# Kernel tuning notes

Hardware: AMD Instinct MI355X
Metric: run time of the kernel (lower is better)

## Reference

```python
import jax, jax.numpy as jnp
import numpy as np

DIM = 1024
HEADS = 16
HEAD_DIM = DIM // HEADS
SCALE = HEADS ** (-0.5)  # NOTE: module scales by heads**-0.5, not head_dim**-0.5


def setup_inputs() -> dict:
    key = jax.random.key(0)
    ks = jax.random.split(key, 5)
    B, N = 4, 2048
    x = jax.random.normal(ks[0], (B, N, DIM), dtype=jnp.float32)
    # qkv: Linear(dim, 3*dim); out: Linear(dim, dim). torch Linear: y = x @ W.T + b
    w_qkv = jax.random.normal(ks[1], (3 * DIM, DIM), dtype=jnp.float32) * (DIM ** -0.5)
    b_qkv = jax.random.normal(ks[2], (3 * DIM,), dtype=jnp.float32) * 0.01
    w_out = jax.random.normal(ks[3], (DIM, DIM), dtype=jnp.float32) * (DIM ** -0.5)
    b_out = jax.random.normal(ks[4], (DIM,), dtype=jnp.float32) * 0.01
    return {"x": x, "w_qkv": w_qkv, "b_qkv": b_qkv, "w_out": w_out, "b_out": b_out}


def reference(x, w_qkv, b_qkv, w_out, b_out):
    B, N, D = x.shape
    qkv = x @ w_qkv.T + b_qkv                       # [B, N, 3D]
    qkv = qkv.reshape(B, N, 3, HEADS, HEAD_DIM)
    qkv = jnp.transpose(qkv, (2, 0, 3, 1, 4))       # [3, B, H, N, hd]
    q, k, v = qkv[0], qkv[1], qkv[2]
    attn = jnp.einsum('bhqd,bhkd->bhqk', q, k) * SCALE
    attn = jax.nn.softmax(attn, axis=-1)
    out = jnp.einsum('bhqk,bhkd->bhqd', attn, v)    # [B, H, N, hd]
    out = jnp.transpose(out, (0, 2, 1, 3)).reshape(B, N, D)
    return out @ w_out.T + b_out
```

## Files before the change

kernel.cpp:

```cpp
#include <hip/hip_runtime.h>
#include <math.h>


typedef float v4f    __attribute__((ext_vector_type(4)));
typedef float f32x16 __attribute__((ext_vector_type(16)));
typedef short s4     __attribute__((ext_vector_type(4)));
typedef short bf8    __attribute__((ext_vector_type(8)));

__device__ __forceinline__ unsigned short bf16r(float f) {
    unsigned int u = __float_as_uint(f);
    u += 0x7FFFu + ((u >> 16) & 1u);
    return (unsigned short)(u >> 16);
}
__device__ __forceinline__ float bf16f(unsigned short h) {
    return __uint_as_float(((unsigned int)h) << 16);
}
__device__ __forceinline__ void split2(float a, float b, unsigned int& hi, unsigned int& lo) {
    const unsigned short ha = bf16r(a), hb = bf16r(b);
    hi = (unsigned int)ha | ((unsigned int)hb << 16);
    lo = (unsigned int)bf16r(a - bf16f(ha)) | ((unsigned int)bf16r(b - bf16f(hb)) << 16);
}

__global__ __launch_bounds__(256) void convert_split(const float* __restrict__ in,
                                                     unsigned short* __restrict__ hi,
                                                     unsigned short* __restrict__ lo,
                                                     int n4) {
    const int i = blockIdx.x * 256 + threadIdx.x;
    if (i >= n4) return;
    v4f xv = ((const v4f*)in)[i];
    s4 h, l;
#pragma unroll
    for (int j = 0; j < 4; ++j) {
        unsigned short hv = bf16r(xv[j]);
        h[j] = (short)hv;
        l[j] = (short)bf16r(xv[j] - bf16f(hv));
    }
    ((s4*)hi)[i] = h;
    ((s4*)lo)[i] = l;
}

#define GEMM_CORE(AHI, ALO, BHI, BLO)                                                      \
    __shared__ unsigned short lAh[4096], lAl[4096], lBh[4096], lBl[4096];                  \
    const int m0 = blockIdx.y * 128;                                                       \
    const int j0 = blockIdx.x * 128;                                                       \
    const int t  = threadIdx.x;                                                            \
    const int kp  = t & 3;                                                                 \
    const int r0  = t >> 2;                                                                \
    const int sks = kp >> 1, skh = kp & 1;                                                 \
    const int l   = t & 63;                                                                \
    const int wid = t >> 6;                                                                \
    const int wm  = wid >> 1, wn = wid & 1;                                                \
    const int l31 = l & 31, lh = l >> 5;                                                   \
    int offA[2][2], offB[2][2];                                                            \
    _Pragma("unroll") for (int im = 0; im < 2; ++im)                                       \
    _Pragma("unroll") for (int ks = 0; ks < 2; ++ks) {                                     \
        const int kpr = ks * 2 + lh;                                                       \
        const int rot = (l31 + 2 * kpr) & 31;                                              \
        offA[im][ks] = ((((wm*2+im)*2+ks)*64) + lh*32 + rot) * 8;                          \
        offB[im][ks] = ((((wn*2+im)*2+ks)*64) + lh*32 + rot) * 8;                          \
    }                                                                                      \
    f32x16 acc[2][2];                                                                      \
    _Pragma("unroll") for (int i = 0; i < 2; ++i)                                          \
    _Pragma("unroll") for (int j = 0; j < 2; ++j)                                          \
    _Pragma("unroll") for (int r = 0; r < 16; ++r) acc[i][j][r] = 0.f;                     \
    for (int kt = 0; kt < 32; ++kt) {                                                      \
        __syncthreads();                                                                   \
        const int kb = kt * 32 + kp * 8;                                                   \
        _Pragma("unroll") for (int hh = 0; hh < 2; ++hh) {                                 \
            const int r  = r0 + hh * 64;                                                   \
            const int sl = (((r >> 5) * 2 + sks) * 64 + skh * 32 + (((r & 31) + 2 * kp) & 31)) * 8; \
            const size_t ga = (size_t)(m0 + r) * 1024 + kb;                                \
            const size_t gb = (size_t)(j0 + r) * 1024 + kb;                                \
            *(bf8*)(lAh + sl) = *(const bf8*)(AHI + ga);                                   \
            *(bf8*)(lAl + sl) = *(const bf8*)(ALO + ga);                                   \
            *(bf8*)(lBh + sl) = *(const bf8*)(BHI + gb);                                   \
            *(bf8*)(lBl + sl) = *(const bf8*)(BLO + gb);                                   \
        }                                                                                  \
        __syncthreads();                                                                   \
        _Pragma("unroll") for (int ks = 0; ks < 2; ++ks) {                                 \
            bf8 ah[2], al2[2], bh[2], bl2[2];                                              \
            _Pragma("unroll") for (int im = 0; im < 2; ++im) {                             \
                ah[im]  = *(const bf8*)(lAh + offA[im][ks]);                               \
                al2[im] = *(const bf8*)(lAl + offA[im][ks]);                               \
                bh[im]  = *(const bf8*)(lBh + offB[im][ks]);                               \
                bl2[im] = *(const bf8*)(lBl + offB[im][ks]);                               \
            }                                                                              \
            _Pragma("unroll") for (int im = 0; im < 2; ++im)                               \
            _Pragma("unroll") for (int jn = 0; jn < 2; ++jn) {                             \
                acc[im][jn] = __builtin_amdgcn_mfma_f32_32x32x16_bf16(ah[im],  bh[jn],  acc[im][jn], 0, 0, 0); \
                acc[im][jn] = __builtin_amdgcn_mfma_f32_32x32x16_bf16(ah[im],  bl2[jn], acc[im][jn], 0, 0, 0); \
                acc[im][jn] = __builtin_amdgcn_mfma_f32_32x32x16_bf16(al2[im], bh[jn],  acc[im][jn], 0, 0, 0); \
            }                                                                              \
        }                                                                                  \
    }

__global__ __launch_bounds__(256) void gemm_qkv(
    const unsigned short* __restrict__ Ahi, const unsigned short* __restrict__ Alo,
    const unsigned short* __restrict__ Bhi, const unsigned short* __restrict__ Blo,
    const float* __restrict__ bias,
    unsigned short* __restrict__ Qhi, unsigned short* __restrict__ Qlo,
    unsigned short* __restrict__ Khi, unsigned short* __restrict__ Klo,
    unsigned short* __restrict__ Vhi, unsigned short* __restrict__ Vlo) {
    GEMM_CORE(Ahi, Alo, Bhi, Blo)
#pragma unroll
    for (int im = 0; im < 2; ++im)
#pragma unroll
        for (int jn = 0; jn < 2; ++jn) {
            const int col   = j0 + wn * 64 + jn * 32 + l31;
            const float bv  = bias[col];
            const int rbase = m0 + wm * 64 + im * 32 + 4 * lh;
            const int which = col >> 10;
            const int hcol  = (col & 1023) >> 6;
            const int dd    = col & 63;
            const int bh    = (rbase >> 11) * 16 + hcol;
            unsigned short* const dh = which == 0 ? Qhi : (which == 1 ? Khi : Vhi);
            unsigned short* const dl = which == 0 ? Qlo : (which == 1 ? Klo : Vlo);
            const float sc = which == 0 ? 0.25f : 1.0f;
            const size_t base = (size_t)bh * 131072 + dd;
#pragma unroll
            for (int reg = 0; reg < 16; ++reg) {
                const int row = rbase + (reg & 3) + 8 * (reg >> 2);
                const int n   = row & 2047;
                const float val = (acc[im][jn][reg] + bv) * sc;
                const unsigned short hv = bf16r(val);
                dh[base + (size_t)n * 64] = hv;
                dl[base + (size_t)n * 64] = bf16r(val - bf16f(hv));
            }
        }
}

__global__ __launch_bounds__(256) void gemm_out(
    const unsigned short* __restrict__ Ahi, const unsigned short* __restrict__ Alo,
    const unsigned short* __restrict__ Bhi, const unsigned short* __restrict__ Blo,
    const float* __restrict__ bias, float* __restrict__ out) {
    GEMM_CORE(Ahi, Alo, Bhi, Blo)
#pragma unroll
    for (int im = 0; im < 2; ++im)
#pragma unroll
        for (int jn = 0; jn < 2; ++jn) {
            const int col   = j0 + wn * 64 + jn * 32 + l31;
            const float bv  = bias[col];
            const int rbase = m0 + wm * 64 + im * 32 + 4 * lh;
#pragma unroll
            for (int reg = 0; reg < 16; ++reg) {
                const int row = rbase + (reg & 3) + 8 * (reg >> 2);
                out[(size_t)row * 1024 + col] = acc[im][jn][reg] + bv;
            }
        }
}

__global__ __launch_bounds__(256, 3) void attn_mfma(
    const unsigned short* __restrict__ Qhi, const unsigned short* __restrict__ Qlo,
    const unsigned short* __restrict__ Khi, const unsigned short* __restrict__ Klo,
    const unsigned short* __restrict__ Vhi, const unsigned short* __restrict__ Vlo,
    unsigned short* __restrict__ Ohi, unsigned short* __restrict__ Olo) {
    __shared__ unsigned short Kh_s[4096], Kl_s[4096], Vh_s[4096], Vl_s[4096];

    const int bh = blockIdx.y;
    const int q0 = blockIdx.x * 128;
    const int t  = threadIdx.x;
    const int w  = t >> 6, l = t & 63, l31 = l & 31, lh = l >> 5;
    const size_t bhbase = (size_t)bh * 131072;

    bf8 qh[4], ql[4];
    {
        const size_t qb = bhbase + (size_t)(q0 + w * 32 + l31) * 64 + lh * 8;
#pragma unroll
        for (int ks = 0; ks < 4; ++ks) {
            qh[ks] = *(const bf8*)(Qhi + qb + ks * 16);
            ql[ks] = *(const bf8*)(Qlo + qb + ks * 16);
        }
    }

    float m_run = -INFINITY, l_run = 0.f;
    f32x16 O0, O1;
#pragma unroll
    for (int r = 0; r < 16; ++r) { O0[r] = 0.f; O1[r] = 0.f; }

    for (int kt = 0; kt < 32; ++kt) {
        const int k0 = kt * 64;
        __syncthreads();
#pragma unroll
        for (int pass = 0; pass < 2; ++pass) {
            const int c = pass * 256 + t;
            {
                const int r = c >> 3, kpc = c & 7;
                const int sl = (((r >> 5) * 8 + kpc) * 32 + (((r & 31) + 2 * kpc) & 31)) * 8;
                const size_t g = bhbase + (size_t)(k0 + r) * 64 + kpc * 8;
                *(bf8*)(Kh_s + sl) = *(const bf8*)(Khi + g);
                *(bf8*)(Kl_s + sl) = *(const bf8*)(Klo + g);
            }
            {
                const int kpc = c >> 6, r = c & 63;
                const int sl = (((r >> 5) * 8 + kpc) * 32 + (((r & 31) + 2 * kpc) & 31)) * 8;
                const size_t g = bhbase + (size_t)(k0 + kpc * 8) * 64 + r;
                bf8 vh, vl;
#pragma unroll
                for (int e = 0; e < 8; ++e) {
                    vh[e] = (short)Vhi[g + e * 64];
                    vl[e] = (short)Vlo[g + e * 64];
                }
                *(bf8*)(Vh_s + sl) = vh;
                *(bf8*)(Vl_s + sl) = vl;
            }
        }
        __syncthreads();

        f32x16 s0, s1;
#pragma unroll
        for (int r = 0; r < 16; ++r) { s0[r] = 0.f; s1[r] = 0.f; }
#pragma unroll
        for (int ks = 0; ks < 4; ++ks) {
            const int kpf = ks * 2 + lh;
            const int rot = (l31 + 2 * kpf) & 31;
            const int b0  = (kpf * 32 + rot) * 8;
            const int b1  = ((8 + kpf) * 32 + rot) * 8;
            const bf8 kh0 = *(const bf8*)(Kh_s + b0), kl0 = *(const bf8*)(Kl_s + b0);
            const bf8 kh1 = *(const bf8*)(Kh_s + b1), kl1 = *(const bf8*)(Kl_s + b1);
            s0 = __builtin_amdgcn_mfma_f32_32x32x16_bf16(kh0, qh[ks], s0, 0, 0, 0);
            s0 = __builtin_amdgcn_mfma_f32_32x32x16_bf16(kh0, ql[ks], s0, 0, 0, 0);
            s0 = __builtin_amdgcn_mfma_f32_32x32x16_bf16(kl0, qh[ks], s0, 0, 0, 0);
            s1 = __builtin_amdgcn_mfma_f32_32x32x16_bf16(kh1, qh[ks], s1, 0, 0, 0);
            s1 = __builtin_amdgcn_mfma_f32_32x32x16_bf16(kh1, ql[ks], s1, 0, 0, 0);
            s1 = __builtin_amdgcn_mfma_f32_32x32x16_bf16(kl1, qh[ks], s1, 0, 0, 0);
        }

        float mx = fmaxf(s0[0], s1[0]);
#pragma unroll
        for (int r = 1; r < 16; ++r) mx = fmaxf(mx, fmaxf(s0[r], s1[r]));
        mx = fmaxf(mx, __shfl_xor(mx, 32));
        const float mn   = fmaxf(m_run, mx);
        const float corr = __expf(m_run - mn);
        m_run = mn;
        float sum = 0.f;
#pragma unroll
        for (int r = 0; r < 16; ++r) {
            s0[r] = __expf(s0[r] - mn); sum += s0[r];
            s1[r] = __expf(s1[r] - mn); sum += s1[r];
        }
        sum += __shfl_xor(sum, 32);
        l_run = l_run * corr + sum;

#pragma unroll
        for (int r = 0; r < 16; ++r) {
            const float cr = __shfl(corr, (r & 3) + 8 * (r >> 2) + 4 * lh);
            O0[r] *= cr; O1[r] *= cr;
        }

#pragma unroll
        for (int ks = 0; ks < 4; ++ks) {
            const int rg = (ks & 1) * 8;
            unsigned int hA0, hA1, hB0, hB1, lA0, lA1, lB0, lB1;
            if (ks < 2) {
                split2(s0[rg + 0], s0[rg + 1], hA0, lA0);
                split2(s0[rg + 2], s0[rg + 3], hA1, lA1);
                split2(s0[rg + 4], s0[rg + 5], hB0, lB0);
                split2(s0[rg + 6], s0[rg + 7], hB1, lB1);
            } else {
                split2(s1[rg + 0], s1[rg + 1], hA0, lA0);
                split2(s1[rg + 2], s1[rg + 3], hA1, lA1);
                split2(s1[rg + 4], s1[rg + 5], hB0, lB0);
                split2(s1[rg + 6], s1[rg + 7], hB1, lB1);
            }
            const unsigned int sh0 = lh ? hA0 : hB0, sh1 = lh ? hA1 : hB1;
            const unsigned int sl0 = lh ? lA0 : lB0, sl1 = lh ? lA1 : lB1;
            const unsigned int rh0 = (unsigned int)__shfl_xor((int)sh0, 32);
            const unsigned int rh1 = (unsigned int)__shfl_xor((int)sh1, 32);
            const unsigned int rl0 = (unsigned int)__shfl_xor((int)sl0, 32);
            const unsigned int rl1 = (unsigned int)__shfl_xor((int)sl1, 32);
            union U { unsigned int u[4]; bf8 v; } ph, pl;
            ph.u[0] = lh ? rh0 : hA0;  ph.u[1] = lh ? rh1 : hA1;
            ph.u[2] = lh ? hB0 : rh0;  ph.u[3] = lh ? hB1 : rh1;
            pl.u[0] = lh ? rl0 : lA0;  pl.u[1] = lh ? rl1 : lA1;
            pl.u[2] = lh ? lB0 : rl0;  pl.u[3] = lh ? lB1 : rl1;

            const int kpf = ks * 2 + lh;
            const int rot = (l31 + 2 * kpf) & 31;
            const int v0  = (kpf * 32 + rot) * 8;
            const int v1  = ((8 + kpf) * 32 + rot) * 8;
            const bf8 vh0 = *(const bf8*)(Vh_s + v0), vl0 = *(const bf8*)(Vl_s + v0);
            const bf8 vh1 = *(const bf8*)(Vh_s + v1), vl1 = *(const bf8*)(Vl_s + v1);
            O0 = __builtin_amdgcn_mfma_f32_32x32x16_bf16(ph.v, vh0, O0, 0, 0, 0);
            O0 = __builtin_amdgcn_mfma_f32_32x32x16_bf16(ph.v, vl0, O0, 0, 0, 0);
            O0 = __builtin_amdgcn_mfma_f32_32x32x16_bf16(pl.v, vh0, O0, 0, 0, 0);
            O1 = __builtin_amdgcn_mfma_f32_32x32x16_bf16(ph.v, vh1, O1, 0, 0, 0);
            O1 = __builtin_amdgcn_mfma_f32_32x32x16_bf16(ph.v, vl1, O1, 0, 0, 0);
            O1 = __builtin_amdgcn_mfma_f32_32x32x16_bf16(pl.v, vh1, O1, 0, 0, 0);
        }
    }

    const int b = bh >> 4, h = bh & 15;
    const float linv_own = 1.f / l_run;
#pragma unroll
    for (int r = 0; r < 16; ++r) {
        const int q = (r & 3) + 8 * (r >> 2) + 4 * lh;
        const float inv = __shfl(linv_own, q);
        const int n = q0 + w * 32 + q;
        const size_t base = ((size_t)b * 2048 + n) * 1024 + h * 64;
        const float v0 = O0[r] * inv, v1 = O1[r] * inv;
        const unsigned short h0 = bf16r(v0), h1 = bf16r(v1);
        Ohi[base + l31]      = h0;  Olo[base + l31]      = bf16r(v0 - bf16f(h0));
        Ohi[base + 32 + l31] = h1;  Olo[base + 32 + l31] = bf16r(v1 - bf16f(h1));
    }
}

extern "C" void kernel_launch(void* const* d_in, const int* in_sizes, int n_in,
                              void* d_out, int out_size, void* d_ws, size_t ws_size,
                              hipStream_t stream) {
    const float* x     = (const float*)d_in[0];
    const float* w_qkv = (const float*)d_in[1];
    const float* b_qkv = (const float*)d_in[2];
    const float* w_out = (const float*)d_in[3];
    const float* b_out = (const float*)d_in[4];
    float* out = (float*)d_out;

    char* ws = (char*)d_ws;
    unsigned short* Qhi = (unsigned short*)ws; ws += (size_t)8388608 * 2;
    unsigned short* Qlo = (unsigned short*)ws; ws += (size_t)8388608 * 2;
    unsigned short* Khi = (unsigned short*)ws; ws += (size_t)8388608 * 2;
    unsigned short* Klo = (unsigned short*)ws; ws += (size_t)8388608 * 2;
    unsigned short* Vhi = (unsigned short*)ws; ws += (size_t)8388608 * 2;
    unsigned short* Vlo = (unsigned short*)ws; ws += (size_t)8388608 * 2;
    unsigned short* Wqh = (unsigned short*)ws; ws += (size_t)3145728 * 2;
    unsigned short* Wql = (unsigned short*)ws; ws += (size_t)3145728 * 2;
    unsigned short* Woh = (unsigned short*)ws; ws += (size_t)1048576 * 2;
    unsigned short* Wol = (unsigned short*)ws; ws += (size_t)1048576 * 2;
    unsigned short* Xhi = (unsigned short*)ws; ws += (size_t)8388608 * 2;
    unsigned short* Xlo = (unsigned short*)ws;
    unsigned short* AThi = Xhi;
    unsigned short* ATlo = Xlo;

    convert_split<<<8192, 256, 0, stream>>>(x,     Xhi, Xlo, 2097152);
    convert_split<<<3072, 256, 0, stream>>>(w_qkv, Wqh, Wql, 786432);
    convert_split<<<1024, 256, 0, stream>>>(w_out, Woh, Wol, 262144);
    gemm_qkv<<<dim3(24, 64), 256, 0, stream>>>(Xhi, Xlo, Wqh, Wql, b_qkv,
                                               Qhi, Qlo, Khi, Klo, Vhi, Vlo);
    attn_mfma<<<dim3(16, 64), 256, 0, stream>>>(Qhi, Qlo, Khi, Klo, Vhi, Vlo, AThi, ATlo);
    gemm_out<<<dim3(8, 64), 256, 0, stream>>>(AThi, ATlo, Woh, Wol, b_out, out);
}
```

Baseline: 626.4 us.

## Store V transposed, skip unneeded softmax rescales, truncate bf16 splits

The QKV GEMM epilogue now writes V in a transposed [bh][d][n] layout with 4-wide vector stores. The attention kernel can then load V tiles with single 16-byte reads instead of eight strided 2-byte gathers. The online softmax rescales O and l only when some lane's running max increases, which saves the shuffles and multiplies on most tiles. The hi/lo bf16 splits now truncate instead of rounding, which is cheaper but slightly less accurate for the lo part.

Measured after the change: 577.6 us. 1.08x faster.

```diff
diff --git a/kernel.cpp b/kernel.cpp
--- a/kernel.cpp
+++ b/kernel.cpp
@@ -15,10 +15,18 @@
 __device__ __forceinline__ float bf16f(unsigned short h) {
     return __uint_as_float(((unsigned int)h) << 16);
 }
-__device__ __forceinline__ void split2(float a, float b, unsigned int& hi, unsigned int& lo) {
-    const unsigned short ha = bf16r(a), hb = bf16r(b);
-    hi = (unsigned int)ha | ((unsigned int)hb << 16);
-    lo = (unsigned int)bf16r(a - bf16f(ha)) | ((unsigned int)bf16r(b - bf16f(hb)) << 16);
+__device__ __forceinline__ void splitt(float v, unsigned short& h, unsigned short& lo2) {
+    const unsigned int u  = __float_as_uint(v);
+    const unsigned int hm = u & 0xFFFF0000u;
+    h   = (unsigned short)(u >> 16);
+    lo2 = (unsigned short)(__float_as_uint(v - __uint_as_float(hm)) >> 16);
+}
+__device__ __forceinline__ void split2t(float a, float b, unsigned int& hi, unsigned int& lo) {
+    const unsigned int ua = __float_as_uint(a), ub = __float_as_uint(b);
+    const unsigned int ha = ua & 0xFFFF0000u,  hb = ub & 0xFFFF0000u;
+    hi = (ha >> 16) | hb;
+    const float la = a - __uint_as_float(ha), lb = b - __uint_as_float(hb);
+    lo = (__float_as_uint(la) >> 16) | (__float_as_uint(lb) & 0xFFFF0000u);
 }
 
 __global__ __launch_bounds__(256) void convert_split(const float* __restrict__ in,
@@ -113,18 +121,36 @@
             const int hcol  = (col & 1023) >> 6;
             const int dd    = col & 63;
             const int bh    = (rbase >> 11) * 16 + hcol;
-            unsigned short* const dh = which == 0 ? Qhi : (which == 1 ? Khi : Vhi);
-            unsigned short* const dl = which == 0 ? Qlo : (which == 1 ? Klo : Vlo);
-            const float sc = which == 0 ? 0.25f : 1.0f;
-            const size_t base = (size_t)bh * 131072 + dd;
-#pragma unroll
-            for (int reg = 0; reg < 16; ++reg) {
-                const int row = rbase + (reg & 3) + 8 * (reg >> 2);
-                const int n   = row & 2047;
-                const float val = (acc[im][jn][reg] + bv) * sc;
-                const unsigned short hv = bf16r(val);
-                dh[base + (size_t)n * 64] = hv;
-                dl[base + (size_t)n * 64] = bf16r(val - bf16f(hv));
+            if (which == 2) {
+                const size_t vbase = (size_t)bh * 131072 + (size_t)dd * 2048 + (rbase & 2047);
+#pragma unroll
+                for (int rq = 0; rq < 4; ++rq) {
+                    s4 hq, lq;
+#pragma unroll
+                    for (int e = 0; e < 4; ++e) {
+                        const float val = acc[im][jn][rq * 4 + e] + bv;
+                        unsigned short hv, lv;
+                        splitt(val, hv, lv);
+                        hq[e] = (short)hv; lq[e] = (short)lv;
+                    }
+                    *(s4*)(Vhi + vbase + 8 * rq) = hq;
+                    *(s4*)(Vlo + vbase + 8 * rq) = lq;
+                }
+            } else {
+                unsigned short* const dh = which == 0 ? Qhi : Khi;
+                unsigned short* const dl = which == 0 ? Qlo : Klo;
+                const float sc = which == 0 ? 0.25f : 1.0f;
+                const size_t base = (size_t)bh * 131072 + dd;
+#pragma unroll
+                for (int reg = 0; reg < 16; ++reg) {
+                    const int row = rbase + (reg & 3) + 8 * (reg >> 2);
+                    const int n   = row & 2047;
+                    const float val = (acc[im][jn][reg] + bv) * sc;
+                    unsigned short hv, lv;
+                    splitt(val, hv, lv);
+                    dh[base + (size_t)n * 64] = hv;
+                    dl[base + (size_t)n * 64] = lv;
+                }
             }
         }
 }
@@ -183,25 +209,17 @@
 #pragma unroll
         for (int pass = 0; pass < 2; ++pass) {
             const int c = pass * 256 + t;
+            const int r = c >> 3, kpc = c & 7;
+            const int sl = (((r >> 5) * 8 + kpc) * 32 + (((r & 31) + 2 * kpc) & 31)) * 8;
             {
-                const int r = c >> 3, kpc = c & 7;
-                const int sl = (((r >> 5) * 8 + kpc) * 32 + (((r & 31) + 2 * kpc) & 31)) * 8;
                 const size_t g = bhbase + (size_t)(k0 + r) * 64 + kpc * 8;
                 *(bf8*)(Kh_s + sl) = *(const bf8*)(Khi + g);
                 *(bf8*)(Kl_s + sl) = *(const bf8*)(Klo + g);
             }
             {
-                const int kpc = c >> 6, r = c & 63;
-                const int sl = (((r >> 5) * 8 + kpc) * 32 + (((r & 31) + 2 * kpc) & 31)) * 8;
-                const size_t g = bhbase + (size_t)(k0 + kpc * 8) * 64 + r;
-                bf8 vh, vl;
-#pragma unroll
-                for (int e = 0; e < 8; ++e) {
-                    vh[e] = (short)Vhi[g + e * 64];
-                    vl[e] = (short)Vlo[g + e * 64];
-                }
-                *(bf8*)(Vh_s + sl) = vh;
-                *(bf8*)(Vl_s + sl) = vl;
+                const size_t g = bhbase + (size_t)r * 2048 + k0 + kpc * 8;
+                *(bf8*)(Vh_s + sl) = *(const bf8*)(Vhi + g);
+                *(bf8*)(Vl_s + sl) = *(const bf8*)(Vlo + g);
             }
         }
         __syncthreads();
@@ -229,38 +247,40 @@
 #pragma unroll
         for (int r = 1; r < 16; ++r) mx = fmaxf(mx, fmaxf(s0[r], s1[r]));
         mx = fmaxf(mx, __shfl_xor(mx, 32));
-        const float mn   = fmaxf(m_run, mx);
-        const float corr = __expf(m_run - mn);
-        m_run = mn;
+        if (__any(mx > m_run)) {
+            const float mn   = fmaxf(m_run, mx);
+            const float corr = __expf(m_run - mn);
+            m_run = mn;
+            l_run *= corr;
+#pragma unroll
+            for (int r = 0; r < 16; ++r) {
+                const float cr = __shfl(corr, (r & 3) + 8 * (r >> 2) + 4 * lh);
+                O0[r] *= cr; O1[r] *= cr;
+            }
+        }
         float sum = 0.f;
 #pragma unroll
         for (int r = 0; r < 16; ++r) {
-            s0[r] = __expf(s0[r] - mn); sum += s0[r];
-            s1[r] = __expf(s1[r] - mn); sum += s1[r];
+            s0[r] = __expf(s0[r] - m_run); sum += s0[r];
+            s1[r] = __expf(s1[r] - m_run); sum += s1[r];
         }
         sum += __shfl_xor(sum, 32);
-        l_run = l_run * corr + sum;
-
-#pragma unroll
-        for (int r = 0; r < 16; ++r) {
-            const float cr = __shfl(corr, (r & 3) + 8 * (r >> 2) + 4 * lh);
-            O0[r] *= cr; O1[r] *= cr;
-        }
+        l_run += sum;
 
 #pragma unroll
         for (int ks = 0; ks < 4; ++ks) {
             const int rg = (ks & 1) * 8;
             unsigned int hA0, hA1, hB0, hB1, lA0, lA1, lB0, lB1;
             if (ks < 2) {
-                split2(s0[rg + 0], s0[rg + 1], hA0, lA0);
-                split2(s0[rg + 2], s0[rg + 3], hA1, lA1);
-                split2(s0[rg + 4], s0[rg + 5], hB0, lB0);
-                split2(s0[rg + 6], s0[rg + 7], hB1, lB1);
+                split2t(s0[rg + 0], s0[rg + 1], hA0, lA0);
+                split2t(s0[rg + 2], s0[rg + 3], hA1, lA1);
+                split2t(s0[rg + 4], s0[rg + 5], hB0, lB0);
+                split2t(s0[rg + 6], s0[rg + 7], hB1, lB1);
             } else {
-                split2(s1[rg + 0], s1[rg + 1], hA0, lA0);
-                split2(s1[rg + 2], s1[rg + 3], hA1, lA1);
-                split2(s1[rg + 4], s1[rg + 5], hB0, lB0);
-                split2(s1[rg + 6], s1[rg + 7], hB1, lB1);
+                split2t(s1[rg + 0], s1[rg + 1], hA0, lA0);
+                split2t(s1[rg + 2], s1[rg + 3], hA1, lA1);
+                split2t(s1[rg + 4], s1[rg + 5], hB0, lB0);
+                split2t(s1[rg + 6], s1[rg + 7], hB1, lB1);
             }
             const unsigned int sh0 = lh ? hA0 : hB0, sh1 = lh ? hA1 : hB1;
             const unsigned int sl0 = lh ? lA0 : lB0, sl1 = lh ? lA1 : lB1;
@@ -298,9 +318,11 @@
         const int n = q0 + w * 32 + q;
         const size_t base = ((size_t)b * 2048 + n) * 1024 + h * 64;
         const float v0 = O0[r] * inv, v1 = O1[r] * inv;
-        const unsigned short h0 = bf16r(v0), h1 = bf16r(v1);
-        Ohi[base + l31]      = h0;  Olo[base + l31]      = bf16r(v0 - bf16f(h0));
-        Ohi[base + 32 + l31] = h1;  Olo[base + 32 + l31] = bf16r(v1 - bf16f(h1));
+        unsigned short h0, l0s, h1, l1s;
+        splitt(v0, h0, l0s);
+        splitt(v1, h1, l1s);
+        Ohi[base + l31]      = h0;  Olo[base + l31]      = l0s;
+        Ohi[base + 32 + l31] = h1;  Olo[base + 32 + l31] = l1s;
     }
 }
 
```
